# Performance work log

Hardware: AMD Instinct MI355X
Metric: run time of the kernel (lower is better)

## Reference

```python
import jax, jax.numpy as jnp
import numpy as np

D = 1024      # embed_dim
H = 16        # attention heads
DH = D // H   # head size
B, S = 8, 1024
EPS = 1e-5


def setup_inputs() -> dict:
    key = jax.random.key(0)
    ks = jax.random.split(key, 12)
    s = lambda fan: 1.0 / np.sqrt(fan)
    return {
        "x":  jax.random.normal(ks[0], (B, S, D), dtype=jnp.float32),
        # per-head projections, stacked: [H, D, DH]
        "Wq": jax.random.normal(ks[1], (H, D, DH), jnp.float32) * s(D),
        "Wk": jax.random.normal(ks[2], (H, D, DH), jnp.float32) * s(D),
        "Wv": jax.random.normal(ks[3], (H, D, DH), jnp.float32) * s(D),
        "Wo": jax.random.normal(ks[4], (D, D), jnp.float32) * s(D),
        "bo": jnp.zeros((D,), jnp.float32),
        "g1": jnp.ones((D,), jnp.float32),
        "b1": jnp.zeros((D,), jnp.float32),
        "W1": jax.random.normal(ks[5], (D, 4 * D), jnp.float32) * s(D),
        "c1": jnp.zeros((4 * D,), jnp.float32),
        "W2": jax.random.normal(ks[6], (4 * D, D), jnp.float32) * s(4 * D),
        "c2": jnp.zeros((D,), jnp.float32),
        "g2": jnp.ones((D,), jnp.float32),
        "b2": jnp.zeros((D,), jnp.float32),
    }


def layer_norm(x, gain, bias):
    # torch uses unbiased variance (ddof=1)
    mean = jnp.mean(x, axis=-1, keepdims=True)
    var = jnp.var(x, axis=-1, keepdims=True, ddof=1)
    return (x - mean) / jnp.sqrt(var + EPS) * gain + bias


def reference(x, Wq, Wk, Wv, Wo, bo, g1, b1, W1, c1, W2, c2, g2, b2):
    # multi-head attention (all heads batched; same math as the per-head loop)
    q = jnp.einsum('bsd,hde->bhse', x, Wq)
    k = jnp.einsum('bsd,hde->bhse', x, Wk)
    v = jnp.einsum('bsd,hde->bhse', x, Wv)
    scores = jnp.einsum('bhse,bhte->bhst', q, k) / jnp.sqrt(jnp.float32(DH))
    attn = jax.nn.softmax(scores, axis=-1)
    ctx = jnp.einsum('bhst,bhte->bhse', attn, v)            # [B,H,S,DH]
    concat = ctx.transpose(0, 2, 1, 3).reshape(B, S, D)     # cat over heads
    attn_out = concat @ Wo + bo
    # residual + LN1
    h = layer_norm(x + attn_out, g1, b1)
    # FFN: Linear -> exact GELU -> Linear (torch nn.GELU default is erf form)
    ff = jax.nn.gelu(h @ W1 + c1, approximate=False) @ W2 + c2
    # residual + LN2
    return layer_norm(h + ff, g2, b2)
```

## Files before the change

kernel.cpp:

```cpp
#include <hip/hip_runtime.h>
#include <hip/hip_bf16.h>
#include <math.h>

typedef unsigned short u16;
typedef unsigned int u32;
typedef __attribute__((ext_vector_type(8))) __bf16 bf16x8;
typedef __attribute__((ext_vector_type(4))) float f32x4;
typedef __attribute__((ext_vector_type(16))) float f32x16;
typedef __attribute__((ext_vector_type(8))) u16 u16x8;
typedef __attribute__((ext_vector_type(4))) u16 u16x4;
typedef __attribute__((ext_vector_type(4))) u32 u32x4;

#define DEV static __device__ __forceinline__

DEV u16 f2bf(float x) {
  __bf16 b = (__bf16)x;
  return __builtin_bit_cast(u16, b);
}
DEV float bf2f(u16 u) {
  unsigned v = ((unsigned)u) << 16;
  return __builtin_bit_cast(float, v);
}

DEV void gl_lds16(const u16* g, u16* l) {
  __builtin_amdgcn_global_load_lds(
      (const __attribute__((address_space(1))) void*)g,
      (__attribute__((address_space(3))) void*)l, 16, 0, 0);
}

DEV float waveRedSum(float v) {
  v += __shfl_xor(v, 1);  v += __shfl_xor(v, 2);  v += __shfl_xor(v, 4);
  v += __shfl_xor(v, 8);  v += __shfl_xor(v, 16); v += __shfl_xor(v, 32);
  return v;
}

DEV float exp2_fast(float x) {
  float r;
  asm("v_exp_f32 %0, %1" : "=v"(r) : "v"(x));
  return r;
}
DEV float vmax16(f32x16 v) {
  float a = fmaxf(v[0], v[1]), b = fmaxf(v[2], v[3]);
  float c = fmaxf(v[4], v[5]), d = fmaxf(v[6], v[7]);
  float e = fmaxf(v[8], v[9]), f = fmaxf(v[10], v[11]);
  float g = fmaxf(v[12], v[13]), h = fmaxf(v[14], v[15]);
  a = fmaxf(a, b); c = fmaxf(c, d); e = fmaxf(e, f); g = fmaxf(g, h);
  return fmaxf(fmaxf(a, c), fmaxf(e, g));
}
DEV float vsum16(f32x16 v) {
  float a = v[0] + v[1], b = v[2] + v[3], c = v[4] + v[5], d = v[6] + v[7];
  float e = v[8] + v[9], f = v[10] + v[11], g = v[12] + v[13], h = v[14] + v[15];
  a += b; c += d; e += f; g += h;
  return (a + c) + (e + g);
}
DEV f32x16 mfma32(bf16x8 a, bf16x8 b, f32x16 c) {
  return __builtin_amdgcn_mfma_f32_32x32x16_bf16(a, b, c, 0, 0, 0);
}
DEV u32 pack2(float lo, float hi2) {
  return ((u32)f2bf(hi2) << 16) | (u32)f2bf(lo);
}
DEV void pack_direct(const f32x16& s, bf16x8* out) {
  u32x4 f0 = {pack2(s[0], s[1]),   pack2(s[2], s[3]),
              pack2(s[4], s[5]),   pack2(s[6], s[7])};
  u32x4 f1 = {pack2(s[8], s[9]),   pack2(s[10], s[11]),
              pack2(s[12], s[13]), pack2(s[14], s[15])};
  out[0] = __builtin_bit_cast(bf16x8, f0);
  out[1] = __builtin_bit_cast(bf16x8, f1);
}

__global__ __launch_bounds__(256)
void cvt_f32_bf16(const float* __restrict__ in, u16* __restrict__ out, int n8) {
  int i = blockIdx.x * 256 + threadIdx.x;
  if (i >= n8) return;
  const float4 a = *(const float4*)(in + (size_t)i * 8);
  const float4 b = *(const float4*)(in + (size_t)i * 8 + 4);
  u16x8 o;
  o[0] = f2bf(a.x); o[1] = f2bf(a.y); o[2] = f2bf(a.z); o[3] = f2bf(a.w);
  o[4] = f2bf(b.x); o[5] = f2bf(b.y); o[6] = f2bf(b.z); o[7] = f2bf(b.w);
  *(u16x8*)(out + (size_t)i * 8) = o;
}

__global__ __launch_bounds__(256)
void pack_wqkv(const float* __restrict__ Wq, const float* __restrict__ Wk,
               const float* __restrict__ Wv, u16* __restrict__ out) {
  __shared__ float tl[64][65];
  int bid = blockIdx.x;
  int which = bid / 256;
  int rem = bid % 256;
  int h = rem / 16, dt = rem % 16;
  const float* W = (which == 0) ? Wq : (which == 1) ? Wk : Wv;
  int t = threadIdx.x, tx = t & 63, ty = t >> 6;
  const float* src = W + (size_t)h * 65536 + (size_t)dt * 64 * 64;
#pragma unroll
  for (int i = 0; i < 16; ++i) {
    int dr = ty * 16 + i;
    tl[dr][tx] = src[(size_t)dr * 64 + tx];
  }
  __syncthreads();
#pragma unroll
  for (int i = 0; i < 16; ++i) {
    int e = ty * 16 + i;
    out[(size_t)(which * 1024 + h * 64 + e) * 1024 + dt * 64 + tx] = f2bf(tl[tx][e]);
  }
}

__global__ __launch_bounds__(256)
void pack_wt(const float* __restrict__ W, u16* __restrict__ out, int K, int N) {
  __shared__ float tl[64][65];
  int ntiles = N >> 6;
  int kt = blockIdx.x / ntiles, nt = blockIdx.x % ntiles;
  int t = threadIdx.x, tx = t & 63, ty = t >> 6;
#pragma unroll
  for (int i = 0; i < 16; ++i) {
    int kr = ty * 16 + i;
    tl[kr][tx] = W[(size_t)(kt * 64 + kr) * N + nt * 64 + tx];
  }
  __syncthreads();
#pragma unroll
  for (int i = 0; i < 16; ++i) {
    int nr = ty * 16 + i;
    out[(size_t)(nt * 64 + nr) * K + kt * 64 + tx] = f2bf(tl[tx][nr]);
  }
}

template <int EPI>
__global__ __launch_bounds__(512, 4)
void gemm256(const u16* __restrict__ A, const u16* __restrict__ Bt,
             void* __restrict__ Cout, const float* __restrict__ bias,
             int M, int N, int K,
             u16* __restrict__ qp_out, u16* __restrict__ kp_out,
             u16* __restrict__ vt_out) {
  constexpr int BM = 128, BN = 256;
  constexpr int SLOT = (BM + BN) * 32;
  __shared__ __align__(16) u16 lds[3 * SLOT];

  const int t = threadIdx.x;
  const int lane = t & 63, w = t >> 6;
  const int li = lane & 15, lg = lane >> 4;
  const int wm = w >> 2, wn = w & 3;

  const int tiles_n = N >> 8;
  const int nwg = gridDim.x;
  const int wgid = (blockIdx.x & 7) * (nwg >> 3) + (blockIdx.x >> 3);
  const int m0 = (wgid / tiles_n) * BM;
  const int n0 = (wgid % tiles_n) << 8;

  const int srow = t >> 2;
  const int scol = (((t & 3) ^ ((t >> 3) & 3)) << 3);
  const u16* aS0 = A  + (size_t)(m0 + srow) * K + scol;
  const u16* bS0 = Bt + (size_t)(n0 + srow) * K + scol;
  const u16* bS1 = Bt + (size_t)(n0 + 128 + srow) * K + scol;
  u16* dWave = &lds[w * 512];

  int aOff[4], bOff[4];
#pragma unroll
  for (int i = 0; i < 4; ++i) {
    int row = wm * 64 + i * 16 + li;
    aOff[i] = row * 32 + ((lg ^ ((row >> 1) & 3)) << 3);
  }
#pragma unroll
  for (int j = 0; j < 4; ++j) {
    int row = wn * 64 + j * 16 + li;
    bOff[j] = BM * 32 + row * 32 + ((lg ^ ((row >> 1) & 3)) << 3);
  }

  f32x4 acc[4][4] = {};
  const int NT = K >> 5;

#define STAGE256(TT, SL)                                             \
  {                                                                  \
    const int kk = (TT) << 5;                                        \
    u16* db = dWave + (SL) * SLOT;                                   \
    gl_lds16(aS0 + kk, db);                                          \
    gl_lds16(bS0 + kk, db + BM * 32);                                \
    gl_lds16(bS1 + kk, db + BM * 32 + 4096);                         \
  }

  STAGE256(0, 0);
  STAGE256(1, 1);

  int so = 0;
  for (int tt = 0; tt < NT; ++tt) {
    if (tt + 1 < NT) asm volatile("s_waitcnt vmcnt(3)" ::: "memory");
    else             asm volatile("s_waitcnt vmcnt(0)" ::: "memory");
    __builtin_amdgcn_s_barrier();
    __builtin_amdgcn_sched_barrier(0);

    int s2 = so + 2; if (s2 >= 3) s2 -= 3;
    if (tt + 2 < NT) STAGE256(tt + 2, s2);

    const u16* sb = &lds[so * SLOT];
    bf16x8 af[4], bfr[4];
#pragma unroll
    for (int i = 0; i < 4; ++i) af[i] = *(const bf16x8*)&sb[aOff[i]];
#pragma unroll
    for (int j = 0; j < 4; ++j) bfr[j] = *(const bf16x8*)&sb[bOff[j]];

    __builtin_amdgcn_s_setprio(1);
#pragma unroll
    for (int i = 0; i < 4; ++i)
#pragma unroll
      for (int j = 0; j < 4; ++j)
        acc[i][j] = __builtin_amdgcn_mfma_f32_16x16x32_bf16(af[i], bfr[j], acc[i][j], 0, 0, 0);
    __builtin_amdgcn_s_setprio(0);

    so = (so + 1 == 3) ? 0 : so + 1;
  }
#undef STAGE256

  if constexpr (EPI == 3) {
    const int which = n0 >> 10;
    const int colb = (n0 & 1023) + wn * 64 + li;
#pragma unroll
    for (int i = 0; i < 4; ++i) {
      const int row0 = m0 + wm * 64 + i * 16 + lg * 4;
      const int bb = row0 >> 10;
      const int s0r = row0 & 1023;
#pragma unroll
      for (int j = 0; j < 4; ++j) {
        const int c = colb + j * 16;
        const int hh = c >> 6, e = c & 63;
        const size_t hb = ((size_t)(bb * 16 + hh)) << 16;
        if (which == 2) {
          u16x4 pk;
#pragma unroll
          for (int r = 0; r < 4; ++r) pk[r] = f2bf(acc[i][j][r]);
          const int s_sw = (s0r & ~12) | ((s0r & 4) << 1) | ((s0r & 8) >> 1);
          *(u16x4*)(vt_out + hb + ((size_t)e << 10) + s_sw) = pk;
        } else {
          u16* dst = (which == 0) ? qp_out : kp_out;
#pragma unroll
          for (int r = 0; r < 4; ++r)
            dst[hb + (size_t)(s0r + r) * 64 + e] = f2bf(acc[i][j][r]);
        }
      }
    }
    return;
  }

  const int colBase = n0 + wn * 64 + li;
#pragma unroll
  for (int i = 0; i < 4; ++i) {
#pragma unroll
    for (int j = 0; j < 4; ++j) {
      int col = colBase + j * 16;
      float bv = bias[col];
#pragma unroll
      for (int r = 0; r < 4; ++r) {
        int row = m0 + wm * 64 + i * 16 + lg * 4 + r;
        float v = acc[i][j][r] + bv;
        if (EPI == 2) v = 0.5f * v * (1.0f + erff(v * 0.70710678118654752f));
        if (EPI == 1) ((float*)Cout)[(size_t)row * N + col] = v;
        else          ((u16*)Cout)[(size_t)row * N + col] = f2bf(v);
      }
    }
  }
}

__global__ __launch_bounds__(256, 2)
void attn32(const u16* __restrict__ qp, const u16* __restrict__ kp,
            const u16* __restrict__ vt, u16* __restrict__ ctx) {
  __shared__ __align__(16) u16 lds[2][2][4096];
  const int t = threadIdx.x, l = t & 63, w = t >> 6;
  const int l31 = l & 31, hi = l >> 5;
  const int bid = blockIdx.x;
  const int idx = bid >> 3;
  const int bh = (bid & 7) * 16 + (idx >> 3);
  const int qt = idx & 7;
  const int b = bh >> 4, h = bh & 15;
  const int qg = qt * 128 + w * 32;
  const size_t base = (size_t)bh << 16;
  const float SC = 0.18033688011112042f;

  const u16* qrow = qp + base + (size_t)(qg + l31) * 64 + 8 * hi;
  bf16x8 qb[4];
#pragma unroll
  for (int f = 0; f < 4; ++f) qb[f] = *(const bf16x8*)(qrow + f * 16);

  const u16* kbh = kp + base;
  const u16* vbh = vt + base;
  const int sl0 = w, sl1 = 4 + w;

#define STAGE_KV(KB, BUF)                                                        \
  {                                                                              \
    u16* KT = &lds[BUF][0][0];                                                   \
    u16* VT = &lds[BUF][1][0];                                                   \
    const u16* ks = kbh + (size_t)(KB) * 4096;                                   \
    const u16* vs = vbh + (KB) * 64;                                             \
    gl_lds16(ks + (size_t)l * 64 + sl0 * 8,   KT + sl0 * 512);                   \
    gl_lds16(ks + (size_t)l * 64 + sl1 * 8,   KT + sl1 * 512);                   \
    gl_lds16(vs + (size_t)l * 1024 + sl0 * 8, VT + sl0 * 512);                   \
    gl_lds16(vs + (size_t)l * 1024 + sl1 * 8, VT + sl1 * 512);                   \
  }

  f32x16 o0 = {}, o1 = {};
  float m_run = -1e30f, l_run = 0.0f;

  STAGE_KV(0, 0);
  __syncthreads();

  int buf = 0;
  for (int kb = 0; kb < 16; ++kb) {
    if (kb < 15) STAGE_KV(kb + 1, buf ^ 1);

    const u16* KT = &lds[buf][0][0];
    const u16* VT = &lds[buf][1][0];

    bf16x8 ka[8];
#pragma unroll
    for (int f = 0; f < 4; ++f) {
      const int s = (2 * f + hi) * 512 + l31 * 8;
      ka[f]     = *(const bf16x8*)&KT[s];
      ka[4 + f] = *(const bf16x8*)&KT[s + 256];
    }

    __builtin_amdgcn_s_setprio(1);
    f32x16 s0 = {}, s1 = {};
#pragma unroll
    for (int f = 0; f < 4; ++f) s0 = mfma32(ka[f], qb[f], s0);
#pragma unroll
    for (int f = 0; f < 4; ++f) s1 = mfma32(ka[4 + f], qb[f], s1);
    __builtin_amdgcn_s_setprio(0);

    bf16x8 va[8];
#pragma unroll
    for (int c = 0; c < 4; ++c) {
      const int s = (2 * c + hi) * 512 + l31 * 8;
      va[c]     = *(const bf16x8*)&VT[s];
      va[4 + c] = *(const bf16x8*)&VT[s + 256];
    }

    s0 *= SC; s1 *= SC;

    float mx = fmaxf(vmax16(s0), vmax16(s1));
    mx = fmaxf(mx, __shfl_xor(mx, 32));

    float mn = fmaxf(m_run, mx);
    float al = exp2_fast(m_run - mn);
    m_run = mn;
    l_run *= al; o0 *= al; o1 *= al;

#pragma unroll
    for (int i = 0; i < 16; ++i) s0[i] = exp2_fast(s0[i] - m_run);
#pragma unroll
    for (int i = 0; i < 16; ++i) s1[i] = exp2_fast(s1[i] - m_run);

    float sm = vsum16(s0) + vsum16(s1);
    sm += __shfl_xor(sm, 32);
    l_run += sm;

    bf16x8 pb[4];
    pack_direct(s0, &pb[0]);
    pack_direct(s1, &pb[2]);

    __builtin_amdgcn_s_setprio(1);
    o0 = mfma32(va[0], pb[0], o0);
    o0 = mfma32(va[1], pb[1], o0);
    o0 = mfma32(va[2], pb[2], o0);
    o0 = mfma32(va[3], pb[3], o0);
    o1 = mfma32(va[4], pb[0], o1);
    o1 = mfma32(va[5], pb[1], o1);
    o1 = mfma32(va[6], pb[2], o1);
    o1 = mfma32(va[7], pb[3], o1);
    __builtin_amdgcn_s_setprio(0);

    __syncthreads();
    buf ^= 1;
  }
#undef STAGE_KV

  float inv = 1.0f / l_run;
  o0 *= inv; o1 *= inv;
  u16* crow = ctx + (size_t)(b * 1024 + qg + l31) * 1024 + h * 64 + 4 * hi;
#pragma unroll
  for (int g = 0; g < 4; ++g) {
    u16x4 p0, p1;
#pragma unroll
    for (int j = 0; j < 4; ++j) { p0[j] = f2bf(o0[g * 4 + j]); p1[j] = f2bf(o1[g * 4 + j]); }
    *(u16x4*)(crow + g * 8) = p0;
    *(u16x4*)(crow + 32 + g * 8) = p1;
  }
}

template <int MODE>
__global__ __launch_bounds__(256)
void ln_kernel(const void* __restrict__ in1v, const u16* __restrict__ in2,
               const float* __restrict__ g, const float* __restrict__ bt,
               void* __restrict__ outv) {
  __shared__ float red[4];
  const int row = blockIdx.x;
  const int t = threadIdx.x;
  const int c = t * 4;
  const size_t base = (size_t)row * 1024 + c;

  float a0, a1, a2, a3;
  {
    u16x4 yb = *(const u16x4*)(in2 + base);
    float y0 = bf2f(yb[0]), y1 = bf2f(yb[1]), y2 = bf2f(yb[2]), y3 = bf2f(yb[3]);
    if (MODE == 0) {
      const float4 x = *(const float4*)((const float*)in1v + base);
      a0 = x.x + y0; a1 = x.y + y1; a2 = x.z + y2; a3 = x.w + y3;
    } else {
      u16x4 xb = *(const u16x4*)((const u16*)in1v + base);
      a0 = bf2f(xb[0]) + y0; a1 = bf2f(xb[1]) + y1;
      a2 = bf2f(xb[2]) + y2; a3 = bf2f(xb[3]) + y3;
    }
  }
  float sum = waveRedSum(a0 + a1 + a2 + a3);
  if ((t & 63) == 0) red[t >> 6] = sum;
  __syncthreads();
  float mean = (red[0] + red[1] + red[2] + red[3]) * (1.0f / 1024.0f);
  __syncthreads();
  float d0 = a0 - mean, d1 = a1 - mean, d2 = a2 - mean, d3 = a3 - mean;
  float sq = waveRedSum(d0 * d0 + d1 * d1 + d2 * d2 + d3 * d3);
  if ((t & 63) == 0) red[t >> 6] = sq;
  __syncthreads();
  float var = (red[0] + red[1] + red[2] + red[3]) * (1.0f / 1023.0f);
  float inv = rsqrtf(var + 1e-5f);
  const float4 gv = *(const float4*)(g + c);
  const float4 bv = *(const float4*)(bt + c);
  float o0 = d0 * inv * gv.x + bv.x;
  float o1 = d1 * inv * gv.y + bv.y;
  float o2 = d2 * inv * gv.z + bv.z;
  float o3 = d3 * inv * gv.w + bv.w;
  if (MODE == 0) {
    u16x4 ob; ob[0] = f2bf(o0); ob[1] = f2bf(o1); ob[2] = f2bf(o2); ob[3] = f2bf(o3);
    *(u16x4*)((u16*)outv + base) = ob;
  } else {
    float4 of; of.x = o0; of.y = o1; of.z = o2; of.w = o3;
    *(float4*)((float*)outv + base) = of;
  }
}

extern "C" void kernel_launch(void* const* d_in, const int* in_sizes, int n_in,
                              void* d_out, int out_size, void* d_ws, size_t ws_size,
                              hipStream_t stream) {
  const float* x  = (const float*)d_in[0];
  const float* Wq = (const float*)d_in[1];
  const float* Wk = (const float*)d_in[2];
  const float* Wv = (const float*)d_in[3];
  const float* Wo = (const float*)d_in[4];
  const float* bo = (const float*)d_in[5];
  const float* g1 = (const float*)d_in[6];
  const float* b1 = (const float*)d_in[7];
  const float* W1 = (const float*)d_in[8];
  const float* c1 = (const float*)d_in[9];
  const float* W2 = (const float*)d_in[10];
  const float* c2 = (const float*)d_in[11];
  const float* g2 = (const float*)d_in[12];
  const float* b2 = (const float*)d_in[13];
  float* out = (float*)d_out;

  char* ws = (char*)d_ws;
  u16* xb     = (u16*)(ws + 0);
  u16* wqkv_b = (u16*)(ws + 16777216);
  u16* wo_b   = (u16*)(ws + 23068672);
  u16* w1_b   = (u16*)(ws + 25165824);
  u16* w2_b   = (u16*)(ws + 33554432);
  char* R1 = ws + 41943040;
  u16*  qpb  = (u16*)(R1);
  u16*  kpb  = (u16*)(R1 + 16777216);
  u16*  vtb  = (u16*)(R1 + 33554432);
  u16*  ctx  = (u16*)(R1 + 50331648);
  u16*  attn = (u16*)(R1 + 67108864);
  u16*  ff1  = (u16*)(R1);
  u16*  ff2  = (u16*)(R1 + 83886080);
  u16*  h_b  = xb;

  cvt_f32_bf16<<<4096, 256, 0, stream>>>(x, xb, 1048576);
  pack_wqkv<<<768, 256, 0, stream>>>(Wq, Wk, Wv, wqkv_b);
  pack_wt<<<256, 256, 0, stream>>>(Wo, wo_b, 1024, 1024);
  pack_wt<<<1024, 256, 0, stream>>>(W1, w1_b, 1024, 4096);
  pack_wt<<<1024, 256, 0, stream>>>(W2, w2_b, 4096, 1024);

  gemm256<3><<<768, 512, 0, stream>>>(xb, wqkv_b, nullptr, nullptr,
                                      8192, 3072, 1024, qpb, kpb, vtb);
  attn32<<<1024, 256, 0, stream>>>(qpb, kpb, vtb, ctx);
  gemm256<4><<<256, 512, 0, stream>>>(ctx, wo_b, attn, bo, 8192, 1024, 1024,
                                      nullptr, nullptr, nullptr);
  ln_kernel<0><<<8192, 256, 0, stream>>>(x, attn, g1, b1, h_b);
  gemm256<2><<<1024, 512, 0, stream>>>(h_b, w1_b, ff1, c1, 8192, 4096, 1024,
                                       nullptr, nullptr, nullptr);
  gemm256<4><<<256, 512, 0, stream>>>(ff1, w2_b, ff2, c2, 8192, 1024, 4096,
                                      nullptr, nullptr, nullptr);
  ln_kernel<1><<<8192, 256, 0, stream>>>(h_b, ff2, g2, b2, out);
}
```

Before: 350.2 us.

## Add 256x256 ping-pong GEMM with interleaved staging for QKV and FFN1

Adds a new GEMM kernel with 256x256 tiles and double-buffered LDS. Its K loop is split into four MFMA quadrants separated by barriers, and the next tile's A/B loads are issued between quadrants so that global-to-LDS staging overlaps compute. The larger tile gives more reuse per loaded byte, and the kernel is used for the QKV projection and the first FFN GEMM. In exchange, occupancy drops to 2 workgroups per CU and the grids are smaller (384 and 512 blocks), which may leave CUs idle or cause tail effects.

New measurement: 362.8 us. 3.6% more time.

```diff
diff --git a/kernel.cpp b/kernel.cpp
--- a/kernel.cpp
+++ b/kernel.cpp
@@ -55,6 +55,9 @@
 }
 DEV f32x16 mfma32(bf16x8 a, bf16x8 b, f32x16 c) {
   return __builtin_amdgcn_mfma_f32_32x32x16_bf16(a, b, c, 0, 0, 0);
+}
+DEV f32x4 mfma16(bf16x8 a, bf16x8 b, f32x4 c) {
+  return __builtin_amdgcn_mfma_f32_16x16x32_bf16(a, b, c, 0, 0, 0);
 }
 DEV u32 pack2(float lo, float hi2) {
   return ((u32)f2bf(hi2) << 16) | (u32)f2bf(lo);
@@ -124,12 +127,199 @@
 }
 
 template <int EPI>
+__global__ __launch_bounds__(512, 2)
+void gemm8p(const u16* __restrict__ A, const u16* __restrict__ Bt,
+            void* __restrict__ Cout, const float* __restrict__ bias,
+            int M, int N, int K,
+            u16* __restrict__ qp_out, u16* __restrict__ kp_out,
+            u16* __restrict__ vt_out) {
+  constexpr int DB = 32768;
+  constexpr int BOFF = 16384;
+  __shared__ __align__(16) u16 lds[2 * DB];
+
+  const int t = threadIdx.x;
+  const int lane = t & 63, w = t >> 6;
+  const int li = lane & 15, lg = lane >> 4;
+  const int wm = w >> 2, wn = w & 3;
+
+  const int tiles_n = N >> 8;
+  const int nwg = gridDim.x;
+  const int wgid = (blockIdx.x & 7) * (nwg >> 3) + (blockIdx.x >> 3);
+  const int m0 = (wgid / tiles_n) << 8;
+  const int n0 = (wgid % tiles_n) << 8;
+
+  const int sr = t >> 3, cs = t & 7;
+  const int kq = (cs ^ sr) & 7;
+  const u16* aSrc = A  + (size_t)(m0 + sr) * K + kq * 8;
+  const u16* bSrc = Bt + (size_t)(n0 + sr) * K + kq * 8;
+  u16* dW = &lds[w * 512];
+
+  int aOf[2][4], bOf[2][2];
+#pragma unroll
+  for (int mh = 0; mh < 2; ++mh)
+#pragma unroll
+    for (int ii = 0; ii < 4; ++ii) {
+      int r = wm * 128 + mh * 64 + ii * 16 + li;
+      aOf[mh][ii] = r * 64 + ((lg ^ r) & 7) * 8;
+    }
+#pragma unroll
+  for (int nh = 0; nh < 2; ++nh)
+#pragma unroll
+    for (int j = 0; j < 2; ++j) {
+      int r = wn * 64 + nh * 32 + j * 16 + li;
+      bOf[nh][j] = BOFF + r * 64 + ((lg ^ r) & 7) * 8;
+    }
+
+  f32x4 acc[8][4] = {};
+  const int NT = K >> 6;
+
+#define STG(MATP, MOFF, H, T, D)                                            \
+  {                                                                         \
+    const u16* s_ = (MATP) + (size_t)((H) * 128) * K + (size_t)(T) * 64;    \
+    u16* d_ = dW + (D) * DB + (MOFF) + (H) * 8192;                          \
+    gl_lds16(s_, d_);                                                       \
+    gl_lds16(s_ + (size_t)64 * K, d_ + 4096);                               \
+  }
+
+#pragma unroll
+  for (int h = 0; h < 2; ++h) { STG(aSrc, 0, h, 0, 0); STG(bSrc, BOFF, h, 0, 0); }
+#pragma unroll
+  for (int h = 0; h < 2; ++h) { STG(aSrc, 0, h, 1, 1); STG(bSrc, BOFF, h, 1, 1); }
+
+  bf16x8 af[8], b0f[4], b1f[4];
+
+  for (int T = 0; T < NT; ++T) {
+    const int d = T & 1;
+    const u16* sa = &lds[d * DB];
+    const bool stg = (T + 2) < NT;
+
+    if (T + 1 < NT) asm volatile("s_waitcnt vmcnt(8)" ::: "memory");
+    else            asm volatile("s_waitcnt vmcnt(0)" ::: "memory");
+    __builtin_amdgcn_s_barrier();
+    __builtin_amdgcn_sched_barrier(0);
+#pragma unroll
+    for (int ii = 0; ii < 4; ++ii) {
+      af[ii]     = *(const bf16x8*)&sa[aOf[0][ii]];
+      af[4 + ii] = *(const bf16x8*)&sa[aOf[0][ii] ^ 32];
+    }
+#pragma unroll
+    for (int j = 0; j < 2; ++j) {
+      b0f[j]     = *(const bf16x8*)&sa[bOf[0][j]];
+      b0f[2 + j] = *(const bf16x8*)&sa[bOf[0][j] ^ 32];
+    }
+    __builtin_amdgcn_s_setprio(1);
+#pragma unroll
+    for (int kh = 0; kh < 2; ++kh)
+#pragma unroll
+      for (int ii = 0; ii < 4; ++ii)
+#pragma unroll
+        for (int j = 0; j < 2; ++j)
+          acc[ii][j] = mfma16(af[kh * 4 + ii], b0f[kh * 2 + j], acc[ii][j]);
+    __builtin_amdgcn_s_setprio(0);
+
+    __builtin_amdgcn_s_barrier();
+    __builtin_amdgcn_sched_barrier(0);
+#pragma unroll
+    for (int j = 0; j < 2; ++j) {
+      b1f[j]     = *(const bf16x8*)&sa[bOf[1][j]];
+      b1f[2 + j] = *(const bf16x8*)&sa[bOf[1][j] ^ 32];
+    }
+    __builtin_amdgcn_s_setprio(1);
+#pragma unroll
+    for (int kh = 0; kh < 2; ++kh)
+#pragma unroll
+      for (int ii = 0; ii < 4; ++ii)
+#pragma unroll
+        for (int j = 0; j < 2; ++j)
+          acc[ii][2 + j] = mfma16(af[kh * 4 + ii], b1f[kh * 2 + j], acc[ii][2 + j]);
+    __builtin_amdgcn_s_setprio(0);
+
+    __builtin_amdgcn_s_barrier();
+    __builtin_amdgcn_sched_barrier(0);
+    if (stg) { STG(bSrc, BOFF, 0, T + 2, d); STG(bSrc, BOFF, 1, T + 2, d); }
+#pragma unroll
+    for (int ii = 0; ii < 4; ++ii) {
+      af[ii]     = *(const bf16x8*)&sa[aOf[1][ii]];
+      af[4 + ii] = *(const bf16x8*)&sa[aOf[1][ii] ^ 32];
+    }
+    __builtin_amdgcn_s_setprio(1);
+#pragma unroll
+    for (int kh = 0; kh < 2; ++kh)
+#pragma unroll
+      for (int ii = 0; ii < 4; ++ii)
+#pragma unroll
+        for (int j = 0; j < 2; ++j)
+          acc[4 + ii][2 + j] = mfma16(af[kh * 4 + ii], b1f[kh * 2 + j], acc[4 + ii][2 + j]);
+    __builtin_amdgcn_s_setprio(0);
+
+    __builtin_amdgcn_s_barrier();
+    __builtin_amdgcn_sched_barrier(0);
+    if (stg) { STG(aSrc, 0, 0, T + 2, d); STG(aSrc, 0, 1, T + 2, d); }
+    __builtin_amdgcn_s_setprio(1);
+#pragma unroll
+    for (int kh = 0; kh < 2; ++kh)
+#pragma unroll
+      for (int ii = 0; ii < 4; ++ii)
+#pragma unroll
+        for (int j = 0; j < 2; ++j)
+          acc[4 + ii][j] = mfma16(af[kh * 4 + ii], b0f[kh * 2 + j], acc[4 + ii][j]);
+    __builtin_amdgcn_s_setprio(0);
+  }
+#undef STG
+
+  if constexpr (EPI == 3) {
+    const int which = n0 >> 10;
+    const int colb = (n0 & 1023) + wn * 64 + li;
+#pragma unroll
+    for (int i = 0; i < 8; ++i) {
+      const int row0 = m0 + wm * 128 + (i >> 2) * 64 + (i & 3) * 16 + lg * 4;
+      const int bb = row0 >> 10;
+      const int s0r = row0 & 1023;
+#pragma unroll
+      for (int j = 0; j < 4; ++j) {
+        const int c = colb + (j >> 1) * 32 + (j & 1) * 16;
+        const int hh = c >> 6, e = c & 63;
+        const size_t hb = ((size_t)(bb * 16 + hh)) << 16;
+        if (which == 2) {
+          u16x4 pk;
+#pragma unroll
+          for (int r = 0; r < 4; ++r) pk[r] = f2bf(acc[i][j][r]);
+          const int s_sw = (s0r & ~12) | ((s0r & 4) << 1) | ((s0r & 8) >> 1);
+          *(u16x4*)(vt_out + hb + ((size_t)e << 10) + s_sw) = pk;
+        } else {
+          u16* dst = (which == 0) ? qp_out : kp_out;
+#pragma unroll
+          for (int r = 0; r < 4; ++r)
+            dst[hb + (size_t)(s0r + r) * 64 + e] = f2bf(acc[i][j][r]);
+        }
+      }
+    }
+    return;
+  }
+
+  const int colBase = n0 + wn * 64 + li;
+#pragma unroll
+  for (int i = 0; i < 8; ++i) {
+#pragma unroll
+    for (int j = 0; j < 4; ++j) {
+      int col = colBase + (j >> 1) * 32 + (j & 1) * 16;
+      float bv = bias[col];
+#pragma unroll
+      for (int r = 0; r < 4; ++r) {
+        int row = m0 + wm * 128 + (i >> 2) * 64 + (i & 3) * 16 + lg * 4 + r;
+        float v = acc[i][j][r] + bv;
+        if (EPI == 2) v = 0.5f * v * (1.0f + erff(v * 0.70710678118654752f));
+        ((u16*)Cout)[(size_t)row * N + col] = f2bf(v);
+      }
+    }
+  }
+}
+
+template <int EPI>
 __global__ __launch_bounds__(512, 4)
 void gemm256(const u16* __restrict__ A, const u16* __restrict__ Bt,
              void* __restrict__ Cout, const float* __restrict__ bias,
-             int M, int N, int K,
-             u16* __restrict__ qp_out, u16* __restrict__ kp_out,
-             u16* __restrict__ vt_out) {
+             int M, int N, int K) {
   constexpr int BM = 128, BN = 256;
   constexpr int SLOT = (BM + BN) * 32;
   __shared__ __align__(16) u16 lds[3 * SLOT];
@@ -201,42 +391,12 @@
     for (int i = 0; i < 4; ++i)
 #pragma unroll
       for (int j = 0; j < 4; ++j)
-        acc[i][j] = __builtin_amdgcn_mfma_f32_16x16x32_bf16(af[i], bfr[j], acc[i][j], 0, 0, 0);
+        acc[i][j] = mfma16(af[i], bfr[j], acc[i][j]);
     __builtin_amdgcn_s_setprio(0);
 
     so = (so + 1 == 3) ? 0 : so + 1;
   }
 #undef STAGE256
-
-  if constexpr (EPI == 3) {
-    const int which = n0 >> 10;
-    const int colb = (n0 & 1023) + wn * 64 + li;
-#pragma unroll
-    for (int i = 0; i < 4; ++i) {
-      const int row0 = m0 + wm * 64 + i * 16 + lg * 4;
-      const int bb = row0 >> 10;
-      const int s0r = row0 & 1023;
-#pragma unroll
-      for (int j = 0; j < 4; ++j) {
-        const int c = colb + j * 16;
-        const int hh = c >> 6, e = c & 63;
-        const size_t hb = ((size_t)(bb * 16 + hh)) << 16;
-        if (which == 2) {
-          u16x4 pk;
-#pragma unroll
-          for (int r = 0; r < 4; ++r) pk[r] = f2bf(acc[i][j][r]);
-          const int s_sw = (s0r & ~12) | ((s0r & 4) << 1) | ((s0r & 8) >> 1);
-          *(u16x4*)(vt_out + hb + ((size_t)e << 10) + s_sw) = pk;
-        } else {
-          u16* dst = (which == 0) ? qp_out : kp_out;
-#pragma unroll
-          for (int r = 0; r < 4; ++r)
-            dst[hb + (size_t)(s0r + r) * 64 + e] = f2bf(acc[i][j][r]);
-        }
-      }
-    }
-    return;
-  }
 
   const int colBase = n0 + wn * 64 + li;
 #pragma unroll
@@ -473,15 +633,13 @@
   pack_wt<<<1024, 256, 0, stream>>>(W1, w1_b, 1024, 4096);
   pack_wt<<<1024, 256, 0, stream>>>(W2, w2_b, 4096, 1024);
 
-  gemm256<3><<<768, 512, 0, stream>>>(xb, wqkv_b, nullptr, nullptr,
-                                      8192, 3072, 1024, qpb, kpb, vtb);
+  gemm8p<3><<<384, 512, 0, stream>>>(xb, wqkv_b, nullptr, nullptr,
+                                     8192, 3072, 1024, qpb, kpb, vtb);
   attn32<<<1024, 256, 0, stream>>>(qpb, kpb, vtb, ctx);
-  gemm256<4><<<256, 512, 0, stream>>>(ctx, wo_b, attn, bo, 8192, 1024, 1024,
-                                      nullptr, nullptr, nullptr);
+  gemm256<4><<<256, 512, 0, stream>>>(ctx, wo_b, attn, bo, 8192, 1024, 1024);
   ln_kernel<0><<<8192, 256, 0, stream>>>(x, attn, g1, b1, h_b);
-  gemm256<2><<<1024, 512, 0, stream>>>(h_b, w1_b, ff1, c1, 8192, 4096, 1024,
-                                       nullptr, nullptr, nullptr);
-  gemm256<4><<<256, 512, 0, stream>>>(ff1, w2_b, ff2, c2, 8192, 1024, 4096,
-                                      nullptr, nullptr, nullptr);
+  gemm8p<2><<<512, 512, 0, stream>>>(h_b, w1_b, ff1, c1, 8192, 4096, 1024,
+                                     nullptr, nullptr, nullptr);
+  gemm256<4><<<256, 512, 0, stream>>>(ff1, w2_b, ff2, c2, 8192, 1024, 4096);
   ln_kernel<1><<<8192, 256, 0, stream>>>(h_b, ff2, g2, b2, out);
 }
```
